# Optimization experiments

Hardware: AMD Instinct MI355X
Metric: run time of the kernel (lower is better)

Reference implementation:

```python
import jax, jax.numpy as jnp
import numpy as np

SIZE = 512
NUM_HEADS = 8
HEAD_SIZE = SIZE // NUM_HEADS
EPS = 1e-5  # GroupNorm default eps


def setup_inputs() -> dict:
    key = jax.random.key(0)
    ks = jax.random.split(key, 8)
    B, T, D = 2, 2048, SIZE
    mk = lambda k: jax.random.normal(k, (D, D), dtype=jnp.float32) / D
    return {
        "x": jax.random.normal(ks[0], (B, T, D), dtype=jnp.float32),
        "W_Q": mk(ks[1]),
        "W_K": mk(ks[2]),
        "W_V": mk(ks[3]),
        "W_G": mk(ks[4]),
        "W_O": mk(ks[5]),
        "gn_weight": jnp.ones((D,), dtype=jnp.float32),
        "gn_bias": jnp.zeros((D,), dtype=jnp.float32),
    }


def _retention(x, W_Q, W_K, W_V):
    B, T, D = x.shape
    H, dh = NUM_HEADS, HEAD_SIZE
    # projections -> (B, H, T, dh)
    q = (x @ W_Q).reshape(B, T, H, dh).transpose(0, 2, 1, 3)
    k = (x @ W_K).reshape(B, T, H, dh).transpose(0, 2, 1, 3)
    v = (x @ W_V).reshape(B, T, H, dh).transpose(0, 2, 1, 3)
    # multi-scale per-head decay: gamma_h = 1 - 2^{-5-h}
    gammas = 1.0 - jnp.exp2(-5.0 - jnp.arange(H, dtype=jnp.float32))
    idx = jnp.arange(T)
    diff = (idx[:, None] - idx[None, :]).astype(jnp.float32)  # (T, T)
    causal = diff >= 0
    # D[h, n, m] = gamma_h^{n-m} for n >= m else 0
    decay = jnp.where(causal[None], jnp.exp(diff[None] * jnp.log(gammas)[:, None, None]), 0.0)
    scores = jnp.einsum("bhtd,bhsd->bhts", q, k) / jnp.sqrt(jnp.float32(dh))
    out = jnp.einsum("bhts,bhsd->bhtd", scores * decay[None], v)
    return out.transpose(0, 2, 1, 3).reshape(B, T, D)


def _group_norm(y, weight, bias):
    # GroupNorm(NUM_HEADS, SIZE) over flattened (B*T, SIZE)
    B, T, D = y.shape
    g = y.reshape(B * T, NUM_HEADS, HEAD_SIZE)
    mean = jnp.mean(g, axis=-1, keepdims=True)
    var = jnp.var(g, axis=-1, keepdims=True)
    g = (g - mean) / jnp.sqrt(var + EPS)
    g = g.reshape(B * T, D) * weight + bias
    return g.reshape(B, T, D)


def reference(x, W_Q, W_K, W_V, W_G, W_O, gn_weight, gn_bias):
    ret = _retention(x, W_Q, W_K, W_V)          # (B, T, D)
    normed = _group_norm(ret, gn_weight, gn_bias)  # (B, T, D)
    return jax.nn.silu(x @ W_G + normed) @ W_O
```

## Files before the change

kernel.cpp:

```cpp
#include <hip/hip_runtime.h>
#include <hip/hip_bf16.h>
#include <math.h>

#define DMODEL 512
#define T_SEQ 2048
#define NH 8
#define DH 64
#define M_ROWS 4096
#define LDST 72

typedef short s16x8 __attribute__((ext_vector_type(8)));
typedef float f32x4 __attribute__((ext_vector_type(4)));

static __device__ __forceinline__ unsigned short f2bf(float f) {
  __hip_bfloat16 h = __float2bfloat16(f);
  return *(unsigned short*)&h;
}
static __device__ __forceinline__ float bf2f(unsigned short u) {
  union { unsigned int i; float f; } x; x.i = (unsigned int)u << 16; return x.f;
}
static __device__ __forceinline__ void gld16(void* lds, const void* g) {
  __builtin_amdgcn_global_load_lds(
      (const __attribute__((address_space(1))) unsigned int*)g,
      (__attribute__((address_space(3))) unsigned int*)lds, 16, 0, 0);
}

__global__ __launch_bounds__(256) void prep_k(
    const float* __restrict__ x, unsigned short* __restrict__ Xb,
    const float* __restrict__ W0, const float* __restrict__ W1,
    const float* __restrict__ W2, const float* __restrict__ W3,
    const float* __restrict__ W4, unsigned short* __restrict__ WT)
{
  __shared__ __align__(16) unsigned short buf[64 * LDST];
  const int bid = blockIdx.x, tid = threadIdx.x;
  if (bid < 1024) {
    const size_t i = ((size_t)bid * 256 + tid) * 8;
    float4 a = *(const float4*)&x[i];
    float4 b = *(const float4*)&x[i + 4];
    s16x8 o;
    o[0]=f2bf(a.x); o[1]=f2bf(a.y); o[2]=f2bf(a.z); o[3]=f2bf(a.w);
    o[4]=f2bf(b.x); o[5]=f2bf(b.y); o[6]=f2bf(b.z); o[7]=f2bf(b.w);
    *(s16x8*)&Xb[i] = o;
    return;
  }
  const int bid2 = bid - 1024;
  const int z = bid2 >> 6, rem = bid2 & 63;
  const int n0 = (rem & 7) * 64, k0 = (rem >> 3) * 64;
  const float* W = (z==0)?W0:(z==1)?W1:(z==2)?W2:(z==3)?W3:W4;
  int rowbase;
  if (z == 0)      rowbase = n0;
  else if (z == 1) rowbase = 512 + (n0 >> 6) * 128;
  else if (z == 2) rowbase = 512 + (n0 >> 6) * 128 + 64;
  else if (z == 3) rowbase = 1536 + n0;
  else             rowbase = 2048 + n0;
  #pragma unroll
  for (int r = 0; r < 4; ++r) {
    int idx = r * 256 + tid;
    int kr = idx >> 4, nc = idx & 15;
    float4 v = *(const float4*)&W[(size_t)(k0 + kr) * DMODEL + n0 + nc * 4];
    buf[(nc*4+0) * LDST + kr] = f2bf(v.x);
    buf[(nc*4+1) * LDST + kr] = f2bf(v.y);
    buf[(nc*4+2) * LDST + kr] = f2bf(v.z);
    buf[(nc*4+3) * LDST + kr] = f2bf(v.w);
  }
  __syncthreads();
  #pragma unroll
  for (int r = 0; r < 2; ++r) {
    int idx = r * 256 + tid;
    int nr = idx >> 3, c = idx & 7;
    *(s16x8*)&WT[((size_t)(rowbase + nr)) * DMODEL + k0 + c * 8] =
        *(const s16x8*)&buf[nr * LDST + c * 8];
  }
}

__global__ __launch_bounds__(256) void proj_kv_k(
    const unsigned short* __restrict__ A, const unsigned short* __restrict__ BT,
    unsigned short* __restrict__ Qb, unsigned short* __restrict__ Kb,
    unsigned short* __restrict__ Vb, unsigned short* __restrict__ Gb,
    float* __restrict__ AT)
{
  __shared__ __align__(16) unsigned short smem[2 * 128 * 64];
  unsigned short* As = smem;
  unsigned short* Bs = smem + 128 * 64;
  const int ng0 = blockIdx.x * 128;
  const int m0 = blockIdx.y * 128;
  const int tid = threadIdx.x;
  const int wave = tid >> 6, lane = tid & 63;
  const int wm = wave >> 1, wn = wave & 1;
  const int n = lane & 15, quad = lane >> 4;

  int srow[4], scol[4];
  #pragma unroll
  for (int r = 0; r < 4; ++r) {
    int idx = r * 256 + tid;
    srow[r] = idx >> 3;
    scol[r] = ((idx & 7) ^ (srow[r] & 7)) * 8;
  }

  f32x4 acc[4][4];
  #pragma unroll
  for (int mi = 0; mi < 4; ++mi)
    #pragma unroll
    for (int ni = 0; ni < 4; ++ni) acc[mi][ni] = (f32x4){0.f,0.f,0.f,0.f};

  for (int k0 = 0; k0 < 512; k0 += 64) {
    #pragma unroll
    for (int r = 0; r < 4; ++r) {
      int idx = r * 256 + tid;
      gld16(&As[idx * 8], &A[(size_t)(m0 + srow[r]) * DMODEL + k0 + scol[r]]);
      gld16(&Bs[idx * 8], &BT[(size_t)(ng0 + srow[r]) * DMODEL + k0 + scol[r]]);
    }
    __syncthreads();
    #pragma unroll
    for (int kk = 0; kk < 2; ++kk) {
      s16x8 af[4], bf[4];
      #pragma unroll
      for (int mi = 0; mi < 4; ++mi) {
        int R = wm*64 + mi*16 + n, cc = (kk*4 + quad) ^ (n & 7);
        af[mi] = *(const s16x8*)&As[R * 64 + cc * 8];
      }
      #pragma unroll
      for (int ni = 0; ni < 4; ++ni) {
        int R = wn*64 + ni*16 + n, cc = (kk*4 + quad) ^ (n & 7);
        bf[ni] = *(const s16x8*)&Bs[R * 64 + cc * 8];
      }
      #pragma unroll
      for (int mi = 0; mi < 4; ++mi)
        #pragma unroll
        for (int ni = 0; ni < 4; ++ni)
          acc[mi][ni] = __builtin_amdgcn_mfma_f32_16x16x32_bf16(
              af[mi], bf[ni], acc[mi][ni], 0, 0, 0);
    }
    __syncthreads();
  }

  const int bx = blockIdx.x;
  if (bx < 4 || bx >= 12) {
    unsigned short* Cz = (bx < 4) ? Qb : Gb;
    const int n0 = (bx < 4) ? ng0 : (ng0 - 1536);
    #pragma unroll
    for (int mi = 0; mi < 4; ++mi)
      #pragma unroll
      for (int ni = 0; ni < 4; ++ni)
        #pragma unroll
        for (int r = 0; r < 4; ++r)
          Cz[(size_t)(m0 + wm*64 + mi*16 + quad*4 + r) * DMODEL +
             n0 + wn*64 + ni*16 + n] = f2bf(acc[mi][ni][r]);
    return;
  }

  const int h = (ng0 - 512) >> 7;
  const float lg = log2f(1.0f - exp2f(-5.0f - (float)h));
  unsigned short* KVo = (wn == 0) ? Kb : Vb;
  #pragma unroll
  for (int mi = 0; mi < 4; ++mi)
    #pragma unroll
    for (int ni = 0; ni < 4; ++ni)
      #pragma unroll
      for (int r = 0; r < 4; ++r)
        KVo[(size_t)(m0 + wm*64 + mi*16 + quad*4 + r) * DMODEL +
            h*DH + ni*16 + n] = f2bf(acc[mi][ni][r]);

  unsigned short* Kt = smem;
  unsigned short* Vt = smem + 64 * LDST;
  #pragma unroll
  for (int cc2 = 0; cc2 < 2; ++cc2) {
    __syncthreads();
    if (wm == cc2) {
      unsigned short* Tt = (wn == 0) ? Kt : Vt;
      #pragma unroll
      for (int mi = 0; mi < 4; ++mi)
        #pragma unroll
        for (int r = 0; r < 4; ++r) {
          int m = mi*16 + quad*4 + r;
          float sc = (wn == 0) ? exp2f((float)(64 - m) * lg) : 1.0f;
          #pragma unroll
          for (int ni = 0; ni < 4; ++ni)
            Tt[(ni*16 + n) * LDST + m] = f2bf(acc[mi][ni][r] * sc);
        }
    }
    __syncthreads();
    f32x4 at[4];
    #pragma unroll
    for (int j = 0; j < 4; ++j) at[j] = (f32x4){0.f,0.f,0.f,0.f};
    #pragma unroll
    for (int kk = 0; kk < 2; ++kk) {
      s16x8 a = *(const s16x8*)&Vt[(wave*16 + n) * LDST + kk*32 + quad*8];
      #pragma unroll
      for (int j = 0; j < 4; ++j) {
        s16x8 bf = *(const s16x8*)&Kt[(j*16 + n) * LDST + kk*32 + quad*8];
        at[j] = __builtin_amdgcn_mfma_f32_16x16x32_bf16(a, bf, at[j], 0, 0, 0);
      }
    }
    const int gr = m0 + cc2 * 64;
    const int bb = gr >> 11, cchunk = (gr & 2047) >> 6;
    float* Ab = AT + (((size_t)(bb * NH + h) * 32 + cchunk) << 12);
    #pragma unroll
    for (int j = 0; j < 4; ++j)
      #pragma unroll
      for (int r = 0; r < 4; ++r)
        Ab[(wave*16 + quad*4 + r) * 64 + j*16 + n] = at[j][r];
  }
}

__global__ __launch_bounds__(256) void ret_o2_k(
    const unsigned short* __restrict__ Qb, const unsigned short* __restrict__ Kb,
    const unsigned short* __restrict__ Vb, const float* __restrict__ AT,
    const unsigned short* __restrict__ Gg, const float* __restrict__ gnw,
    const float* __restrict__ gnb, unsigned short* __restrict__ Sb)
{
  __shared__ __align__(16) unsigned short Qs[64 * LDST];
  __shared__ __align__(16) unsigned short Ks[64 * LDST];
  __shared__ __align__(16) unsigned short Vst[64 * LDST];
  __shared__ __align__(16) unsigned short Ss[64 * LDST];
  __shared__ __align__(16) unsigned short Ps[64 * LDST];
  const int c = (int)gridDim.x - 1 - (int)blockIdx.x;
  const int h = blockIdx.y, b = blockIdx.z;
  const int bh = b * NH + h;
  const int tid = threadIdx.x;
  const int wave = tid >> 6, lane = tid & 63;
  const int n = lane & 15, quad = lane >> 4;
  const size_t base = ((size_t)b * T_SEQ + (size_t)c * 64) * DMODEL + h * DH;
  const float lg = log2f(1.0f - exp2f(-5.0f - (float)h));
  const float g64 = exp2f(64.0f * lg);

  #pragma unroll
  for (int r = 0; r < 2; ++r) {
    int idx = r * 256 + tid;
    int i = idx >> 3, ch = idx & 7;
    *(s16x8*)&Qs[i * LDST + ch * 8] =
        *(const s16x8*)&Qb[base + (size_t)i * DMODEL + ch * 8];
    *(s16x8*)&Ks[i * LDST + ch * 8] =
        *(const s16x8*)&Kb[base + (size_t)i * DMODEL + ch * 8];
  }
  #pragma unroll
  for (int r = 0; r < 2; ++r) {
    int idx = r * 256 + tid;
    int m = idx & 63, ch = idx >> 6;
    s16x8 vv = *(const s16x8*)&Vb[base + (size_t)m * DMODEL + ch * 8];
    #pragma unroll
    for (int e = 0; e < 8; ++e)
      Vst[(ch * 8 + e) * LDST + m] = ((unsigned short*)&vv)[e];
  }

  const float* Ac = AT + (((size_t)bh * 32) << 12) + (size_t)tid * 16;
  float4 S0 = {0,0,0,0}, S1 = S0, S2 = S0, S3 = S0;
  if (c > 0) {
    float4 n0 = *(const float4*)(Ac + 0);
    float4 n1 = *(const float4*)(Ac + 4);
    float4 n2 = *(const float4*)(Ac + 8);
    float4 n3 = *(const float4*)(Ac + 12);
    for (int cp = 0; cp < c; ++cp) {
      float4 a0 = n0, a1 = n1, a2 = n2, a3 = n3;
      if (cp + 1 < c) {
        const float* p = Ac + ((size_t)(cp + 1) << 12);
        n0 = *(const float4*)(p + 0);  n1 = *(const float4*)(p + 4);
        n2 = *(const float4*)(p + 8);  n3 = *(const float4*)(p + 12);
      }
      S0.x = fmaf(g64, S0.x, a0.x); S0.y = fmaf(g64, S0.y, a0.y);
      S0.z = fmaf(g64, S0.z, a0.z); S0.w = fmaf(g64, S0.w, a0.w);
      S1.x = fmaf(g64, S1.x, a1.x); S1.y = fmaf(g64, S1.y, a1.y);
      S1.z = fmaf(g64, S1.z, a1.z); S1.w = fmaf(g64, S1.w, a1.w);
      S2.x = fmaf(g64, S2.x, a2.x); S2.y = fmaf(g64, S2.y, a2.y);
      S2.z = fmaf(g64, S2.z, a2.z); S2.w = fmaf(g64, S2.w, a2.w);
      S3.x = fmaf(g64, S3.x, a3.x); S3.y = fmaf(g64, S3.y, a3.y);
      S3.z = fmaf(g64, S3.z, a3.z); S3.w = fmaf(g64, S3.w, a3.w);
    }
  }
  {
    const int d2 = tid >> 2, d1b = (tid & 3) * 16;
    s16x8 lo, hi;
    lo[0]=f2bf(S0.x); lo[1]=f2bf(S0.y); lo[2]=f2bf(S0.z); lo[3]=f2bf(S0.w);
    lo[4]=f2bf(S1.x); lo[5]=f2bf(S1.y); lo[6]=f2bf(S1.z); lo[7]=f2bf(S1.w);
    hi[0]=f2bf(S2.x); hi[1]=f2bf(S2.y); hi[2]=f2bf(S2.z); hi[3]=f2bf(S2.w);
    hi[4]=f2bf(S3.x); hi[5]=f2bf(S3.y); hi[6]=f2bf(S3.z); hi[7]=f2bf(S3.w);
    *(s16x8*)&Ss[d2 * LDST + d1b] = lo;
    *(s16x8*)&Ss[d2 * LDST + d1b + 8] = hi;
  }
  __syncthreads();

  f32x4 s[4], u[4];
  #pragma unroll
  for (int j = 0; j < 4; ++j) {
    s[j] = (f32x4){0.f,0.f,0.f,0.f};
    u[j] = (f32x4){0.f,0.f,0.f,0.f};
  }
  #pragma unroll
  for (int kk = 0; kk < 2; ++kk) {
    s16x8 a = *(const s16x8*)&Qs[(wave*16 + n) * LDST + kk*32 + quad*8];
    #pragma unroll
    for (int j = 0; j < 4; ++j) {
      s16x8 bk = *(const s16x8*)&Ks[(j*16 + n) * LDST + kk*32 + quad*8];
      s[j] = __builtin_amdgcn_mfma_f32_16x16x32_bf16(a, bk, s[j], 0, 0, 0);
      s16x8 bs = *(const s16x8*)&Ss[(j*16 + n) * LDST + kk*32 + quad*8];
      u[j] = __builtin_amdgcn_mfma_f32_16x16x32_bf16(a, bs, u[j], 0, 0, 0);
    }
  }

  float rowf[4], colf[4];
  #pragma unroll
  for (int r = 0; r < 4; ++r) rowf[r] = exp2f((float)(wave*16 + quad*4 + r) * lg);
  #pragma unroll
  for (int j = 0; j < 4; ++j) colf[j] = exp2f(-(float)(j*16 + n) * lg);

  #pragma unroll
  for (int j = 0; j < 4; ++j)
    #pragma unroll
    for (int r = 0; r < 4; ++r) {
      int i = wave*16 + quad*4 + r, mcol = j*16 + n;
      float v = (mcol <= i) ? s[j][r] * 0.125f * rowf[r] * colf[j] : 0.0f;
      Ps[i * LDST + mcol] = f2bf(v);
    }
  __syncthreads();

  f32x4 acc[4];
  #pragma unroll
  for (int j = 0; j < 4; ++j) acc[j] = (f32x4){0.f,0.f,0.f,0.f};
  #pragma unroll
  for (int kk = 0; kk < 2; ++kk) {
    s16x8 a = *(const s16x8*)&Ps[(wave*16 + n) * LDST + kk*32 + quad*8];
    #pragma unroll
    for (int j = 0; j < 4; ++j) {
      s16x8 bf = *(const s16x8*)&Vst[(j*16 + n) * LDST + kk*32 + quad*8];
      acc[j] = __builtin_amdgcn_mfma_f32_16x16x32_bf16(a, bf, acc[j], 0, 0, 0);
    }
  }

  float ov[4][4];
  #pragma unroll
  for (int j = 0; j < 4; ++j)
    #pragma unroll
    for (int r = 0; r < 4; ++r)
      ov[j][r] = acc[j][r] + 0.125f * rowf[r] * u[j][r];

  float gw[4], gb[4];
  #pragma unroll
  for (int j = 0; j < 4; ++j) {
    gw[j] = gnw[h*DH + j*16 + n];
    gb[j] = gnb[h*DH + j*16 + n];
  }

  #pragma unroll
  for (int r = 0; r < 4; ++r) {
    float sum = ov[0][r] + ov[1][r] + ov[2][r] + ov[3][r];
    float sq  = ov[0][r]*ov[0][r] + ov[1][r]*ov[1][r]
              + ov[2][r]*ov[2][r] + ov[3][r]*ov[3][r];
    #pragma unroll
    for (int off = 8; off > 0; off >>= 1) {
      sum += __shfl_xor(sum, off, 64);
      sq  += __shfl_xor(sq,  off, 64);
    }
    const float mean = sum * (1.0f / 64.0f);
    float var = sq * (1.0f / 64.0f) - mean * mean;
    var = fmaxf(var, 0.0f);
    const float rstd = rsqrtf(var + 1e-5f);
    const size_t rowoff = base + (size_t)(wave*16 + quad*4 + r) * DMODEL;
    #pragma unroll
    for (int j = 0; j < 4; ++j) {
      float normed = (ov[j][r] - mean) * rstd * gw[j] + gb[j];
      float uu = bf2f(Gg[rowoff + j*16 + n]) + normed;
      Sb[rowoff + j*16 + n] = f2bf(uu / (1.0f + expf(-uu)));
    }
  }
}

__global__ __launch_bounds__(256) void out_gemm_k(
    const unsigned short* __restrict__ A, const unsigned short* __restrict__ BT,
    float* __restrict__ out)
{
  __shared__ __align__(16) unsigned short As[128 * 64];
  __shared__ __align__(16) unsigned short Bs[64 * 64];
  const int n0 = blockIdx.x * 64;
  const int m0 = blockIdx.y * 128;
  const int tid = threadIdx.x;
  const int wave = tid >> 6, lane = tid & 63;
  const int wm = wave >> 1, wn = wave & 1;
  const int n = lane & 15, quad = lane >> 4;

  int srow[4], scol[4];
  #pragma unroll
  for (int r = 0; r < 4; ++r) {
    int idx = r * 256 + tid;
    srow[r] = idx >> 3;
    scol[r] = ((idx & 7) ^ (srow[r] & 7)) * 8;
  }

  f32x4 acc[4][2];
  #pragma unroll
  for (int mi = 0; mi < 4; ++mi)
    #pragma unroll
    for (int ni = 0; ni < 2; ++ni) acc[mi][ni] = (f32x4){0.f,0.f,0.f,0.f};

  for (int k0 = 0; k0 < 512; k0 += 64) {
    #pragma unroll
    for (int r = 0; r < 4; ++r) {
      int idx = r * 256 + tid;
      gld16(&As[idx * 8], &A[(size_t)(m0 + srow[r]) * DMODEL + k0 + scol[r]]);
    }
    #pragma unroll
    for (int r = 0; r < 2; ++r) {
      int idx = r * 256 + tid;
      gld16(&Bs[idx * 8], &BT[(size_t)(n0 + srow[r]) * DMODEL + k0 + scol[r]]);
    }
    __syncthreads();
    #pragma unroll
    for (int kk = 0; kk < 2; ++kk) {
      s16x8 af[4], bf[2];
      #pragma unroll
      for (int mi = 0; mi < 4; ++mi) {
        int R = wm*64 + mi*16 + n, cc = (kk*4 + quad) ^ (n & 7);
        af[mi] = *(const s16x8*)&As[R * 64 + cc * 8];
      }
      #pragma unroll
      for (int ni = 0; ni < 2; ++ni) {
        int R = wn*32 + ni*16 + n, cc = (kk*4 + quad) ^ (n & 7);
        bf[ni] = *(const s16x8*)&Bs[R * 64 + cc * 8];
      }
      #pragma unroll
      for (int mi = 0; mi < 4; ++mi)
        #pragma unroll
        for (int ni = 0; ni < 2; ++ni)
          acc[mi][ni] = __builtin_amdgcn_mfma_f32_16x16x32_bf16(
              af[mi], bf[ni], acc[mi][ni], 0, 0, 0);
    }
    __syncthreads();
  }

  #pragma unroll
  for (int mi = 0; mi < 4; ++mi)
    #pragma unroll
    for (int ni = 0; ni < 2; ++ni)
      #pragma unroll
      for (int r = 0; r < 4; ++r)
        out[(size_t)(m0 + wm*64 + mi*16 + quad*4 + r) * DMODEL +
            n0 + wn*32 + ni*16 + n] = acc[mi][ni][r];
}

extern "C" void kernel_launch(void* const* d_in, const int* in_sizes, int n_in,
                              void* d_out, int out_size, void* d_ws, size_t ws_size,
                              hipStream_t stream) {
  const float* x   = (const float*)d_in[0];
  const float* WQ  = (const float*)d_in[1];
  const float* WK  = (const float*)d_in[2];
  const float* WV  = (const float*)d_in[3];
  const float* WG  = (const float*)d_in[4];
  const float* WO  = (const float*)d_in[5];
  const float* gnw = (const float*)d_in[6];
  const float* gnb = (const float*)d_in[7];
  float* out = (float*)d_out;

  char* ws = (char*)d_ws;
  unsigned short* Xb = (unsigned short*)(ws);
  unsigned short* Qb = (unsigned short*)(ws + 4  * (1<<20));
  unsigned short* Kb = (unsigned short*)(ws + 8  * (1<<20));
  unsigned short* Vb = (unsigned short*)(ws + 12 * (1<<20));
  unsigned short* G  = (unsigned short*)(ws + 16 * (1<<20));
  float* AT  = (float*)(ws + 24 * (1<<20));
  unsigned short* Sb = (unsigned short*)(ws + 32 * (1<<20));
  unsigned short* WT = (unsigned short*)(ws + 40 * (1<<20));
  (void)ws_size;

  prep_k<<<dim3(1024 + 320), 256, 0, stream>>>(x, Xb, WQ, WK, WV, WG, WO, WT);
  proj_kv_k<<<dim3(16, M_ROWS / 128), 256, 0, stream>>>(
      Xb, WT, Qb, Kb, Vb, G, AT);
  ret_o2_k<<<dim3(T_SEQ / 64, NH, 2), 256, 0, stream>>>(
      Qb, Kb, Vb, AT, G, gnw, gnb, Sb);
  out_gemm_k<<<dim3(8, M_ROWS / 128), 256, 0, stream>>>(
      Sb, WT + 2048 * DMODEL, out);
}
```

Measured before the change: 125.5 us.

## Stage GEMM and retention epilogues through LDS for vectorized global stores

```diff
diff --git a/kernel.cpp b/kernel.cpp
--- a/kernel.cpp
+++ b/kernel.cpp
@@ -8,6 +8,7 @@
 #define DH 64
 #define M_ROWS 4096
 #define LDST 72
+#define EPST 136
 
 typedef short s16x8 __attribute__((ext_vector_type(8)));
 typedef float f32x4 __attribute__((ext_vector_type(4)));
@@ -79,7 +80,7 @@
     unsigned short* __restrict__ Vb, unsigned short* __restrict__ Gb,
     float* __restrict__ AT)
 {
-  __shared__ __align__(16) unsigned short smem[2 * 128 * 64];
+  __shared__ __align__(16) unsigned short smem[128 * EPST];
   unsigned short* As = smem;
   unsigned short* Bs = smem + 128 * 64;
   const int ng0 = blockIdx.x * 128;
@@ -134,32 +135,42 @@
     __syncthreads();
   }
 
+  unsigned short* Ep = smem;
+  #pragma unroll
+  for (int mi = 0; mi < 4; ++mi)
+    #pragma unroll
+    for (int ni = 0; ni < 4; ++ni)
+      #pragma unroll
+      for (int r = 0; r < 4; ++r)
+        Ep[(wm*64 + mi*16 + quad*4 + r) * EPST + wn*64 + ni*16 + n] =
+            f2bf(acc[mi][ni][r]);
+  __syncthreads();
+
   const int bx = blockIdx.x;
   if (bx < 4 || bx >= 12) {
     unsigned short* Cz = (bx < 4) ? Qb : Gb;
     const int n0 = (bx < 4) ? ng0 : (ng0 - 1536);
     #pragma unroll
-    for (int mi = 0; mi < 4; ++mi)
-      #pragma unroll
-      for (int ni = 0; ni < 4; ++ni)
-        #pragma unroll
-        for (int r = 0; r < 4; ++r)
-          Cz[(size_t)(m0 + wm*64 + mi*16 + quad*4 + r) * DMODEL +
-             n0 + wn*64 + ni*16 + n] = f2bf(acc[mi][ni][r]);
+    for (int t = 0; t < 8; ++t) {
+      int idx = t * 256 + tid;
+      int row = idx >> 4, u = idx & 15;
+      *(s16x8*)&Cz[(size_t)(m0 + row) * DMODEL + n0 + u * 8] =
+          *(const s16x8*)&Ep[row * EPST + u * 8];
+    }
     return;
   }
 
   const int h = (ng0 - 512) >> 7;
   const float lg = log2f(1.0f - exp2f(-5.0f - (float)h));
-  unsigned short* KVo = (wn == 0) ? Kb : Vb;
-  #pragma unroll
-  for (int mi = 0; mi < 4; ++mi)
-    #pragma unroll
-    for (int ni = 0; ni < 4; ++ni)
-      #pragma unroll
-      for (int r = 0; r < 4; ++r)
-        KVo[(size_t)(m0 + wm*64 + mi*16 + quad*4 + r) * DMODEL +
-            h*DH + ni*16 + n] = f2bf(acc[mi][ni][r]);
+  #pragma unroll
+  for (int t = 0; t < 4; ++t) {
+    int idx = t * 256 + tid;
+    int row = idx >> 3, u = idx & 7;
+    *(s16x8*)&Kb[(size_t)(m0 + row) * DMODEL + h*DH + u * 8] =
+        *(const s16x8*)&Ep[row * EPST + u * 8];
+    *(s16x8*)&Vb[(size_t)(m0 + row) * DMODEL + h*DH + u * 8] =
+        *(const s16x8*)&Ep[row * EPST + 64 + u * 8];
+  }
 
   unsigned short* Kt = smem;
   unsigned short* Vt = smem + 64 * LDST;
@@ -209,8 +220,8 @@
     const unsigned short* __restrict__ Gg, const float* __restrict__ gnw,
     const float* __restrict__ gnb, unsigned short* __restrict__ Sb)
 {
-  __shared__ __align__(16) unsigned short Qs[64 * LDST];
-  __shared__ __align__(16) unsigned short Ks[64 * LDST];
+  __shared__ __align__(16) unsigned short Qs[64 * 64];
+  __shared__ __align__(16) unsigned short Ks[64 * 64];
   __shared__ __align__(16) unsigned short Vst[64 * LDST];
   __shared__ __align__(16) unsigned short Ss[64 * LDST];
   __shared__ __align__(16) unsigned short Ps[64 * LDST];
@@ -227,11 +238,9 @@
   #pragma unroll
   for (int r = 0; r < 2; ++r) {
     int idx = r * 256 + tid;
-    int i = idx >> 3, ch = idx & 7;
-    *(s16x8*)&Qs[i * LDST + ch * 8] =
-        *(const s16x8*)&Qb[base + (size_t)i * DMODEL + ch * 8];
-    *(s16x8*)&Ks[i * LDST + ch * 8] =
-        *(const s16x8*)&Kb[base + (size_t)i * DMODEL + ch * 8];
+    int row = idx >> 3, sc = ((idx & 7) ^ (row & 7)) * 8;
+    gld16(&Qs[idx * 8], &Qb[base + (size_t)row * DMODEL + sc]);
+    gld16(&Ks[idx * 8], &Kb[base + (size_t)row * DMODEL + sc]);
   }
   #pragma unroll
   for (int r = 0; r < 2; ++r) {
@@ -285,14 +294,16 @@
     s[j] = (f32x4){0.f,0.f,0.f,0.f};
     u[j] = (f32x4){0.f,0.f,0.f,0.f};
   }
+  const int RA = wave*16 + n;
   #pragma unroll
   for (int kk = 0; kk < 2; ++kk) {
-    s16x8 a = *(const s16x8*)&Qs[(wave*16 + n) * LDST + kk*32 + quad*8];
+    s16x8 a = *(const s16x8*)&Qs[RA * 64 + (((kk*4 + quad) ^ (RA & 7)) * 8)];
     #pragma unroll
     for (int j = 0; j < 4; ++j) {
-      s16x8 bk = *(const s16x8*)&Ks[(j*16 + n) * LDST + kk*32 + quad*8];
+      int RB = j*16 + n;
+      s16x8 bk = *(const s16x8*)&Ks[RB * 64 + (((kk*4 + quad) ^ (RB & 7)) * 8)];
       s[j] = __builtin_amdgcn_mfma_f32_16x16x32_bf16(a, bk, s[j], 0, 0, 0);
-      s16x8 bs = *(const s16x8*)&Ss[(j*16 + n) * LDST + kk*32 + quad*8];
+      s16x8 bs = *(const s16x8*)&Ss[RB * LDST + kk*32 + quad*8];
       u[j] = __builtin_amdgcn_mfma_f32_16x16x32_bf16(a, bs, u[j], 0, 0, 0);
     }
   }
@@ -313,12 +324,19 @@
     }
   __syncthreads();
 
+  #pragma unroll
+  for (int r = 0; r < 2; ++r) {
+    int idx = r * 256 + tid;
+    int row = idx >> 3, sc = ((idx & 7) ^ (row & 7)) * 8;
+    gld16(&Qs[idx * 8], &Gg[base + (size_t)row * DMODEL + sc]);
+  }
+
   f32x4 acc[4];
   #pragma unroll
   for (int j = 0; j < 4; ++j) acc[j] = (f32x4){0.f,0.f,0.f,0.f};
   #pragma unroll
   for (int kk = 0; kk < 2; ++kk) {
-    s16x8 a = *(const s16x8*)&Ps[(wave*16 + n) * LDST + kk*32 + quad*8];
+    s16x8 a = *(const s16x8*)&Ps[RA * LDST + kk*32 + quad*8];
     #pragma unroll
     for (int j = 0; j < 4; ++j) {
       s16x8 bf = *(const s16x8*)&Vst[(j*16 + n) * LDST + kk*32 + quad*8];
@@ -340,6 +358,7 @@
     gb[j] = gnb[h*DH + j*16 + n];
   }
 
+  float normed[4][4];
   #pragma unroll
   for (int r = 0; r < 4; ++r) {
     float sum = ov[0][r] + ov[1][r] + ov[2][r] + ov[3][r];
@@ -354,13 +373,31 @@
     float var = sq * (1.0f / 64.0f) - mean * mean;
     var = fmaxf(var, 0.0f);
     const float rstd = rsqrtf(var + 1e-5f);
-    const size_t rowoff = base + (size_t)(wave*16 + quad*4 + r) * DMODEL;
+    #pragma unroll
+    for (int j = 0; j < 4; ++j)
+      normed[j][r] = (ov[j][r] - mean) * rstd * gw[j] + gb[j];
+  }
+
+  __syncthreads();
+
+  #pragma unroll
+  for (int r = 0; r < 4; ++r) {
+    const int i = wave*16 + quad*4 + r;
     #pragma unroll
     for (int j = 0; j < 4; ++j) {
-      float normed = (ov[j][r] - mean) * rstd * gw[j] + gb[j];
-      float uu = bf2f(Gg[rowoff + j*16 + n]) + normed;
-      Sb[rowoff + j*16 + n] = f2bf(uu / (1.0f + expf(-uu)));
-    }
+      const int col = j*16 + n;
+      const int gidx = i * 64 + (((col >> 3) ^ (i & 7)) * 8) + (col & 7);
+      float uu = bf2f(Qs[gidx]) + normed[j][r];
+      Ps[i * LDST + col] = f2bf(uu / (1.0f + expf(-uu)));
+    }
+  }
+  __syncthreads();
+  #pragma unroll
+  for (int t = 0; t < 2; ++t) {
+    int idx = t * 256 + tid;
+    int row = idx >> 3, u8 = idx & 7;
+    *(s16x8*)&Sb[base + (size_t)row * DMODEL + u8 * 8] =
+        *(const s16x8*)&Ps[row * LDST + u8 * 8];
   }
 }
 
```

After: 126.1 us. Within noise of the previous version (+0.4%).
